# Kernel optimization log

Measured on AMD Instinct MI355X. Metric: run time of the kernel, lower is better.

The kernel has to match this reference:

```python
import jax, jax.numpy as jnp
import numpy as np

D_ATOM, D_MODEL, H = 128, 512, 4
D_H = D_ATOM // H
D_FF = 4 * D_ATOM
EPS = 1e-5


def _ln(x, g, b):
    m = jnp.mean(x, axis=-1, keepdims=True)
    v = jnp.mean((x - m) ** 2, axis=-1, keepdims=True)
    return (x - m) / jnp.sqrt(v + EPS) * g + b


def setup_inputs() -> dict:
    key = jax.random.key(0)
    ks = jax.random.split(key, 20)
    B, N_ATOM, N_PAIRS, N_TOK = 2, 2048, 16384, 512
    c_atom = jax.random.normal(ks[0], (B, N_ATOM, D_ATOM), dtype=jnp.float32)
    p_lm = jax.random.normal(ks[1], (B, N_PAIRS, 16), dtype=jnp.float32)
    p_lm_idx = jax.random.randint(ks[2], (B, N_PAIRS, 2), 0, N_ATOM, dtype=jnp.int32)
    token_idx = jnp.sort(jax.random.randint(ks[3], (B, N_ATOM), 0, N_TOK, dtype=jnp.int32), axis=-1)
    s = 0.05
    w = lambda k, sh: jax.random.normal(k, sh, dtype=jnp.float32) * s
    return {
        'c_atom': c_atom, 'p_lm': p_lm, 'p_lm_idx': p_lm_idx,
        'token_idx': token_idx, 'n_tokens': N_TOK,
        'ln_attn_g': jnp.ones((D_ATOM,), jnp.float32), 'ln_attn_b': jnp.zeros((D_ATOM,), jnp.float32),
        'w_q': w(ks[4], (D_ATOM, D_ATOM)), 'w_k': w(ks[5], (D_ATOM, D_ATOM)),
        'w_v': w(ks[6], (D_ATOM, D_ATOM)), 'w_g': w(ks[7], (D_ATOM, D_ATOM)),
        'w_o': w(ks[8], (D_ATOM, D_ATOM)),
        'pb_w': w(ks[9], (16, H)), 'pb_b': jnp.zeros((H,), jnp.float32),
        'ln_ff_g': jnp.ones((D_ATOM,), jnp.float32), 'ln_ff_b': jnp.zeros((D_ATOM,), jnp.float32),
        'sw_w1': w(ks[10], (D_ATOM, D_FF)), 'sw_w2': w(ks[11], (D_ATOM, D_FF)),
        'sw_w3': w(ks[12], (D_FF, D_ATOM)),
        'tok_w': w(ks[13], (D_ATOM, D_MODEL)), 'tok_b': jnp.zeros((D_MODEL,), jnp.float32),
    }


def reference(c_atom, p_lm, p_lm_idx, token_idx, n_tokens,
              ln_attn_g, ln_attn_b, w_q, w_k, w_v, w_g, w_o, pb_w, pb_b,
              ln_ff_g, ln_ff_b, sw_w1, sw_w2, sw_w3, tok_w, tok_b):
    B, N, _ = c_atom.shape
    q_n = _ln(c_atom, ln_attn_g, ln_attn_b)
    Q = (q_n @ w_q).reshape(B, N, H, D_H)
    K = (q_n @ w_k).reshape(B, N, H, D_H)
    V = (q_n @ w_v).reshape(B, N, H, D_H)
    G = q_n @ w_g  # (B, N, d_atom)

    scores = jnp.einsum('bihd,bjhd->bhij', Q, K) / jnp.sqrt(jnp.float32(D_H))

    bias = p_lm @ pb_w + pb_b  # (B, P, H)
    def scat(src, dst, b_):
        return jnp.zeros((H, N, N), b_.dtype).at[:, src, dst].set(b_.T)
    pair_bias = jax.vmap(scat)(p_lm_idx[..., 0], p_lm_idx[..., 1], bias)
    scores = scores + pair_bias

    token_mask = token_idx[:, :, None] == token_idx[:, None, :]  # (B,N,N)
    scores = jnp.where(token_mask[:, None], scores, -jnp.inf)
    attn = jax.nn.softmax(scores, axis=-1)
    attn = jnp.nan_to_num(attn)

    att_out = jnp.einsum('bhij,bjhd->bihd', attn, V).reshape(B, N, D_ATOM)
    q = c_atom + jax.nn.sigmoid(G) * (att_out @ w_o)
    h = _ln(q, ln_ff_g, ln_ff_b)
    q = q + (jax.nn.silu(h @ sw_w1) * (h @ sw_w2)) @ sw_w3
    atom_feat = q @ tok_w + tok_b  # (B, N, d_model)

    seg = (token_idx + jnp.arange(B, dtype=token_idx.dtype)[:, None] * n_tokens).reshape(-1)
    sums = jax.ops.segment_sum(atom_feat.reshape(B * N, D_MODEL), seg, num_segments=B * n_tokens)
    cnts = jax.ops.segment_sum(jnp.ones((B * N,), atom_feat.dtype), seg, num_segments=B * n_tokens)
    out = sums / jnp.maximum(cnts, 1.0)[:, None]
    return out.reshape(B, n_tokens, D_MODEL)
```

## Files before the change

kernel.cpp:

```cpp
#include <hip/hip_runtime.h>
#include <hip/hip_bf16.h>
#include <math.h>

#define B_     2
#define N_     2048
#define DA     128
#define H_     4
#define DH     32
#define DFF    512
#define DM     512
#define NT     512
#define NP     16384
#define MAXL   32
#define LDSP   136
#define PVS    40

typedef short bf16x8 __attribute__((ext_vector_type(8)));
typedef float f32x4  __attribute__((ext_vector_type(4)));

__device__ __forceinline__ short bf16r(float x) {
    union { float f; unsigned u; } v; v.f = x;
    unsigned r = v.u + 0x7FFFu + ((v.u >> 16) & 1u);
    return (short)(r >> 16);
}
__device__ __forceinline__ float bf2f(short h) {
    union { unsigned u; float f; } v;
    v.u = ((unsigned)(unsigned short)h) << 16;
    return v.f;
}

__global__ __launch_bounds__(1024) void setup_kernel(
        const float* __restrict__ wq, const float* __restrict__ wk,
        const float* __restrict__ wv, const float* __restrict__ wg,
        const float* __restrict__ wo, const float* __restrict__ w1,
        const float* __restrict__ w2, const float* __restrict__ w3,
        const float* __restrict__ tw, const int* __restrict__ tok,
        const int* __restrict__ pidx,
        const float* __restrict__ c_atom, const float* __restrict__ lng,
        const float* __restrict__ lnb,
        short* __restrict__ pqkvg, short* __restrict__ pwo,
        short* __restrict__ pw12, short* __restrict__ pw3,
        short* __restrict__ ptok, short* __restrict__ hln,
        int* __restrict__ cnt, int* __restrict__ tst,
        int* __restrict__ win) {
    __shared__ int c[1024];
    __shared__ int sb[1024];
    if (blockIdx.x < 42) {
        int gid = blockIdx.x * 1024 + threadIdx.x;
        int lane = gid & 63;
        int grp = gid >> 6;
        int quad = lane >> 4, nn = lane & 15;
        const float* src; short* dst; int stride;
        if (grp < 128) {
            int g = grp; int kt = g & 3, nt = g >> 2;
            int n = nt * 16 + nn;
            const float* w = (n < 128) ? wq : (n < 256) ? wk : (n < 384) ? wv : wg;
            src = w + (kt * 32 + quad * 8) * 128 + (n & 127);
            dst = pqkvg + (g * 64 + lane) * 8;
            stride = 128;
        } else if (grp < 160) {
            int g = grp - 128; int kt = g & 3, nt = g >> 2;
            src = wo + (kt * 32 + quad * 8) * 128 + nt * 16 + nn;
            dst = pwo + (g * 64 + lane) * 8;
            stride = 128;
        } else if (grp < 416) {
            int g = grp - 160; int kt = g & 3, nt = g >> 2;
            int n = nt * 16 + nn;
            src = ((n & 1) ? w2 : w1) + (kt * 32 + quad * 8) * 512 + (n >> 1);
            dst = pw12 + (g * 64 + lane) * 8;
            stride = 512;
        } else if (grp < 544) {
            int g = grp - 416; int kt = g & 15, nt = g >> 4;
            src = w3 + (kt * 32 + quad * 8) * 128 + nt * 16 + nn;
            dst = pw3 + (g * 64 + lane) * 8;
            stride = 128;
        } else {
            int g = grp - 544; int kt = g & 3, nt = g >> 2;
            src = tw + (kt * 32 + quad * 8) * 512 + nt * 16 + nn;
            dst = ptok + (g * 64 + lane) * 8;
            stride = 512;
        }
#pragma unroll
        for (int j = 0; j < 8; j++) dst[j] = bf16r(src[j * stride]);
    } else if (blockIdx.x == 42) {
        int tid = threadIdx.x;
        c[tid] = 0;
        __syncthreads();
#pragma unroll
        for (int i = 0; i < 4; i++) {
            int idx = tid + i * 1024;
            int b = idx >> 11;
            atomicAdd(&c[b * NT + tok[idx]], 1);
        }
        __syncthreads();
        int t = tid & (NT - 1);
        int v = c[tid];
        int* cur = c;
        int* alt = sb;
        for (int d = 1; d < NT; d <<= 1) {
            int y = cur[tid];
            if (t >= d) y += cur[tid - d];
            alt[tid] = y;
            __syncthreads();
            int* tmp = cur; cur = alt; alt = tmp;
        }
        tst[tid] = cur[tid] - v;
        cnt[tid] = v;
    } else if (blockIdx.x < 75) {
        int p = (blockIdx.x - 43) * 1024 + threadIdx.x;
        int b = p >> 14, pp = p & (NP - 1);
        int src = pidx[p * 2], dst = pidx[p * 2 + 1];
        if (tok[b * N_ + src] == tok[b * N_ + dst])
            atomicMax(&win[(b * N_ + src) * MAXL + (dst & 31)], pp + 1);
    } else {
        int t = threadIdx.x;
        int rowg = (blockIdx.x - 75) * 256 + (t >> 2);
        int sub = t & 3;
        const float* xr = c_atom + rowg * DA + sub * 32;
        float4 v[8];
        float s = 0.f, sq = 0.f;
#pragma unroll
        for (int i = 0; i < 8; i++) {
            v[i] = *(const float4*)(xr + i * 4);
            s  += v[i].x + v[i].y + v[i].z + v[i].w;
            sq += v[i].x * v[i].x + v[i].y * v[i].y + v[i].z * v[i].z + v[i].w * v[i].w;
        }
        s += __shfl_xor(s, 1); sq += __shfl_xor(sq, 1);
        s += __shfl_xor(s, 2); sq += __shfl_xor(sq, 2);
        float mean = s * (1.f / 128.f);
        float var = sq * (1.f / 128.f) - mean * mean;
        float inv = rsqrtf(var + 1e-5f);
        const float* gp = lng + sub * 32;
        const float* bp = lnb + sub * 32;
        short* dst = hln + rowg * DA + sub * 32;
#pragma unroll
        for (int i = 0; i < 8; i++) {
            dst[i * 4 + 0] = bf16r((v[i].x - mean) * inv * gp[i * 4 + 0] + bp[i * 4 + 0]);
            dst[i * 4 + 1] = bf16r((v[i].y - mean) * inv * gp[i * 4 + 1] + bp[i * 4 + 1]);
            dst[i * 4 + 2] = bf16r((v[i].z - mean) * inv * gp[i * 4 + 2] + bp[i * 4 + 2]);
            dst[i * 4 + 3] = bf16r((v[i].w - mean) * inv * gp[i * 4 + 3] + bp[i * 4 + 3]);
        }
    }
}

template<int KT, int KTB, int NTT, int STR>
__device__ __forceinline__ void gemm_a(const short* __restrict__ Abase,
                                       const short* __restrict__ Bp,
                                       int nt0, int lane, f32x4* acc) {
    const short* arow = Abase + (lane & 15) * STR + (lane >> 4) * 8;
    const short* bbase = Bp + lane * 8;
#pragma unroll
    for (int kt = 0; kt < KT; kt++) {
        bf16x8 a = *(const bf16x8*)(arow + kt * 32);
#pragma unroll
        for (int nt = 0; nt < NTT; nt++) {
            bf16x8 b = *(const bf16x8*)(bbase + ((nt0 + nt) * KTB + kt) * 512);
            acc[nt] = __builtin_amdgcn_mfma_f32_16x16x32_bf16(a, b, acc[nt], 0, 0, 0);
        }
    }
}

__global__ __launch_bounds__(256, 2) void tokfused(
        const short* __restrict__ hln, const float* __restrict__ c_atom,
        const float* __restrict__ plm,
        const int* __restrict__ tst, const int* __restrict__ cnt,
        const int* __restrict__ win,
        const short* __restrict__ pqkvg, const short* __restrict__ pwo,
        const short* __restrict__ pw12, const short* __restrict__ pw3,
        const short* __restrict__ ptok,
        const float* __restrict__ pbw, const float* __restrict__ pbb,
        const float* __restrict__ lnfg, const float* __restrict__ lnfb,
        const float* __restrict__ tb, float* __restrict__ out) {
    __shared__ __align__(16) char arena[54272];
    short* As  = (short*)(arena + 0);
    short* Qs  = (short*)(arena + 8704);
    short* Ps  = (short*)(arena + 8704);
    short* Ks  = (short*)(arena + 18944);
    short* VT  = (short*)(arena + 27648);
    float* sgf = (float*)(arena + 37888);
    float* valf = (float*)(arena + 8704);
    short* us   = (short*)(arena + 27648);
    short* q2s  = (short*)(arena + 0);
    short* mrs  = (short*)(arena + 25088);

    int token = blockIdx.x;
    int b = token >> 9;
    int tid = threadIdx.x;
    int lane = tid & 63, wave = tid >> 6;
    int quad = lane >> 4, cc = lane & 15;
    int start = tst[token];
    int L = cnt[token]; if (L > MAXL) L = MAXL;

    {
        int row = tid >> 3, sub = tid & 7;
        int4 v0 = {0,0,0,0}, v1 = {0,0,0,0};
        if (row < L) {
            const int4* src = (const int4*)(hln + (size_t)(b * N_ + start + row) * DA + sub * 16);
            v0 = src[0]; v1 = src[1];
        }
        int4* dst = (int4*)(As + row * LDSP + sub * 16);
        dst[0] = v0; dst[1] = v1;
    }
    __syncthreads();

    {
        f32x4 a0[8], a1[8];
#pragma unroll
        for (int i = 0; i < 8; i++)
#pragma unroll
            for (int r = 0; r < 4; r++) { a0[i][r] = 0.f; a1[i][r] = 0.f; }
        gemm_a<4, 4, 8, LDSP>(As, pqkvg, wave * 8, lane, a0);
        gemm_a<4, 4, 8, LDSP>(As + 16 * LDSP, pqkvg, wave * 8, lane, a1);
#pragma unroll
        for (int rt = 0; rt < 2; rt++) {
            f32x4* ac = rt ? a1 : a0;
#pragma unroll
            for (int nt = 0; nt < 8; nt++) {
                int lc = nt * 16 + cc;
#pragma unroll
                for (int r = 0; r < 4; r++) {
                    int lrow = rt * 16 + quad * 4 + r;
                    float v = ac[nt][r];
                    if (wave == 3)      sgf[lrow * 128 + lc] = 1.f / (1.f + expf(-v));
                    else if (wave == 0) Qs[lrow * LDSP + lc] = bf16r(v);
                    else if (wave == 1) Ks[lrow * LDSP + lc] = bf16r(v);
                    else VT[(lc >> 5) * 32 * PVS + (lc & 31) * PVS + lrow] = bf16r(v);
                }
            }
        }
    }
    __syncthreads();

    {
        int h = wave;
        const float scale = 0.17677669529663687f;
        int rb = lane & 15;
        bf16x8 qa0 = *(const bf16x8*)(Qs + rb * LDSP + h * 32 + quad * 8);
        bf16x8 qa1 = *(const bf16x8*)(Qs + (16 + rb) * LDSP + h * 32 + quad * 8);
        bf16x8 kb0 = *(const bf16x8*)(Ks + rb * LDSP + h * 32 + quad * 8);
        bf16x8 kb1 = *(const bf16x8*)(Ks + (16 + rb) * LDSP + h * 32 + quad * 8);
        f32x4 z = {0.f, 0.f, 0.f, 0.f};
        f32x4 sc[2][2];
        sc[0][0] = __builtin_amdgcn_mfma_f32_16x16x32_bf16(qa0, kb0, z, 0, 0, 0);
        sc[0][1] = __builtin_amdgcn_mfma_f32_16x16x32_bf16(qa0, kb1, z, 0, 0, 0);
        sc[1][0] = __builtin_amdgcn_mfma_f32_16x16x32_bf16(qa1, kb0, z, 0, 0, 0);
        sc[1][1] = __builtin_amdgcn_mfma_f32_16x16x32_bf16(qa1, kb1, z, 0, 0, 0);
        __syncthreads();
        short* Ph = Ps + h * 32 * PVS;
        int j0 = cc, j1 = 16 + cc;
#pragma unroll
        for (int it = 0; it < 2; it++) {
#pragma unroll
            for (int r = 0; r < 4; r++) {
                int i = it * 16 + quad * 4 + r;
                int at = start + i; if (at > N_ - 1) at = N_ - 1;
                const int* wrow = win + (size_t)(b * N_ + at) * MAXL;
                float s0 = sc[it][0][r] * scale;
                float s1 = sc[it][1][r] * scale;
                int pw0 = (j0 < L) ? wrow[(start + j0) & 31] : 0;
                int pw1 = (j1 < L) ? wrow[(start + j1) & 31] : 0;
                if (pw0 > 0) {
                    const float* pl = plm + (size_t)(b * NP + pw0 - 1) * 16;
                    float bs = pbb[h];
#pragma unroll
                    for (int f = 0; f < 16; f++) bs += pl[f] * pbw[f * H_ + h];
                    s0 += bs;
                }
                if (pw1 > 0) {
                    const float* pl = plm + (size_t)(b * NP + pw1 - 1) * 16;
                    float bs = pbb[h];
#pragma unroll
                    for (int f = 0; f < 16; f++) bs += pl[f] * pbw[f * H_ + h];
                    s1 += bs;
                }
                if (j0 >= L) s0 = -1e30f;
                if (j1 >= L) s1 = -1e30f;
                float m = fmaxf(s0, s1);
                m = fmaxf(m, __shfl_xor(m, 1));
                m = fmaxf(m, __shfl_xor(m, 2));
                m = fmaxf(m, __shfl_xor(m, 4));
                m = fmaxf(m, __shfl_xor(m, 8));
                float e0 = expf(s0 - m), e1 = expf(s1 - m);
                float sm = e0 + e1;
                sm += __shfl_xor(sm, 1);
                sm += __shfl_xor(sm, 2);
                sm += __shfl_xor(sm, 4);
                sm += __shfl_xor(sm, 8);
                float inv = 1.f / sm;
                Ph[i * PVS + j0] = bf16r(e0 * inv);
                Ph[i * PVS + j1] = bf16r(e1 * inv);
            }
        }
        __syncthreads();
        const short* Vh = VT + h * 32 * PVS;
        bf16x8 va0 = *(const bf16x8*)(Vh + rb * PVS + quad * 8);
        bf16x8 va1 = *(const bf16x8*)(Vh + (16 + rb) * PVS + quad * 8);
        bf16x8 pb0 = *(const bf16x8*)(Ph + rb * PVS + quad * 8);
        bf16x8 pb1 = *(const bf16x8*)(Ph + (16 + rb) * PVS + quad * 8);
        f32x4 ot[2][2];
        ot[0][0] = __builtin_amdgcn_mfma_f32_16x16x32_bf16(va0, pb0, z, 0, 0, 0);
        ot[0][1] = __builtin_amdgcn_mfma_f32_16x16x32_bf16(va0, pb1, z, 0, 0, 0);
        ot[1][0] = __builtin_amdgcn_mfma_f32_16x16x32_bf16(va1, pb0, z, 0, 0, 0);
        ot[1][1] = __builtin_amdgcn_mfma_f32_16x16x32_bf16(va1, pb1, z, 0, 0, 0);
#pragma unroll
        for (int dt = 0; dt < 2; dt++)
#pragma unroll
            for (int itile = 0; itile < 2; itile++)
#pragma unroll
                for (int r = 0; r < 4; r++)
                    As[(itile * 16 + cc) * LDSP + h * 32 + dt * 16 + quad * 4 + r] =
                        bf16r(ot[dt][itile][r]);
    }
    __syncthreads();

    {
        f32x4 a3[4];
#pragma unroll
        for (int i = 0; i < 4; i++)
#pragma unroll
            for (int r = 0; r < 4; r++) a3[i][r] = 0.f;
        gemm_a<4, 4, 4, LDSP>(As + (wave >> 1) * 16 * LDSP, pwo, (wave & 1) * 4, lane, a3);
#pragma unroll
        for (int ntl = 0; ntl < 4; ntl++) {
            int gcol = ((wave & 1) * 4 + ntl) * 16 + cc;
#pragma unroll
            for (int r = 0; r < 4; r++) {
                int lrow = (wave >> 1) * 16 + quad * 4 + r;
                int garow = start + lrow; if (garow > N_ - 1) garow = N_ - 1;
                float v = c_atom[(size_t)(b * N_ + garow) * DA + gcol]
                        + sgf[lrow * 128 + gcol] * a3[ntl][r];
                valf[lrow * 128 + gcol] = v;
            }
        }
    }
    __syncthreads();

    {
        int row = tid >> 3, sub = tid & 7;
        const float* vr = valf + row * 128 + sub * 16;
        float4 x[4];
        float s = 0.f, sq = 0.f;
#pragma unroll
        for (int i = 0; i < 4; i++) {
            x[i] = *(const float4*)(vr + i * 4);
            s  += x[i].x + x[i].y + x[i].z + x[i].w;
            sq += x[i].x * x[i].x + x[i].y * x[i].y + x[i].z * x[i].z + x[i].w * x[i].w;
        }
        s += __shfl_xor(s, 1); sq += __shfl_xor(sq, 1);
        s += __shfl_xor(s, 2); sq += __shfl_xor(sq, 2);
        s += __shfl_xor(s, 4); sq += __shfl_xor(sq, 4);
        float mean = s * (1.f / 128.f);
        float var = sq * (1.f / 128.f) - mean * mean;
        float inv = rsqrtf(var + 1e-5f);
        short* hr = As + row * LDSP + sub * 16;
        const float* gp = lnfg + sub * 16;
        const float* bp = lnfb + sub * 16;
#pragma unroll
        for (int i = 0; i < 4; i++) {
            hr[i * 4 + 0] = bf16r((x[i].x - mean) * inv * gp[i * 4 + 0] + bp[i * 4 + 0]);
            hr[i * 4 + 1] = bf16r((x[i].y - mean) * inv * gp[i * 4 + 1] + bp[i * 4 + 1]);
            hr[i * 4 + 2] = bf16r((x[i].z - mean) * inv * gp[i * 4 + 2] + bp[i * 4 + 2]);
            hr[i * 4 + 3] = bf16r((x[i].w - mean) * inv * gp[i * 4 + 3] + bp[i * 4 + 3]);
        }
    }
    __syncthreads();

    f32x4 c3a[4];
#pragma unroll
    for (int i = 0; i < 4; i++)
#pragma unroll
        for (int r = 0; r < 4; r++) c3a[i][r] = 0.f;
#pragma unroll
    for (int ch = 0; ch < 2; ch++) {
        f32x4 u0[8], u1[8];
#pragma unroll
        for (int i = 0; i < 8; i++)
#pragma unroll
            for (int r = 0; r < 4; r++) { u0[i][r] = 0.f; u1[i][r] = 0.f; }
        const short* bp12 = pw12 + ch * 32 * 4 * 512;
        gemm_a<4, 4, 8, LDSP>(As, bp12, wave * 8, lane, u0);
        gemm_a<4, 4, 8, LDSP>(As + 16 * LDSP, bp12, wave * 8, lane, u1);
#pragma unroll
        for (int rt = 0; rt < 2; rt++) {
            f32x4* ac = rt ? u1 : u0;
#pragma unroll
            for (int nt = 0; nt < 8; nt++) {
                int col8 = (wave * 8 + nt) * 8 + (cc >> 1);
#pragma unroll
                for (int r = 0; r < 4; r++) {
                    float v = ac[nt][r];
                    float p = __shfl_xor(v, 1);
                    if (!(lane & 1)) {
                        float sil = v / (1.f + expf(-v));
                        us[(rt * 16 + quad * 4 + r) * 264 + col8] = bf16r(sil * p);
                    }
                }
            }
        }
        __syncthreads();
        gemm_a<8, 16, 4, 264>(us + (wave >> 1) * 16 * 264, pw3 + ch * 8 * 512,
                              (wave & 1) * 4, lane, c3a);
        __syncthreads();
    }

    {
#pragma unroll
        for (int ntl = 0; ntl < 4; ntl++) {
            int gcol = ((wave & 1) * 4 + ntl) * 16 + cc;
#pragma unroll
            for (int r = 0; r < 4; r++) {
                int lrow = (wave >> 1) * 16 + quad * 4 + r;
                q2s[lrow * 128 + gcol] = bf16r(valf[lrow * 128 + gcol] + c3a[ntl][r]);
            }
        }
    }
    __syncthreads();

    if (tid < 128) {
        int col = tid;
        float sum = 0.f;
        for (int i = 0; i < L; i++) sum += bf2f(q2s[i * 128 + col]);
        float inv = (L > 0) ? 1.f / (float)L : 0.f;
        mrs[col] = bf16r(sum * inv);
    }
    __syncthreads();

    {
        f32x4 a8[8];
#pragma unroll
        for (int i = 0; i < 8; i++)
#pragma unroll
            for (int r = 0; r < 4; r++) a8[i][r] = 0.f;
        gemm_a<4, 4, 8, LDSP>(mrs, ptok, wave * 8, lane, a8);
        if (quad == 0) {
#pragma unroll
            for (int nt = 0; nt < 8; nt++) {
                int col = (wave * 8 + nt) * 16 + cc;
                out[(size_t)token * DM + col] = a8[nt][0] + tb[col];
            }
        }
    }
}

extern "C" void kernel_launch(void* const* d_in, const int* in_sizes, int n_in,
                              void* d_out, int out_size, void* d_ws, size_t ws_size,
                              hipStream_t stream) {
    const float* c_atom  = (const float*)d_in[0];
    const float* p_lm    = (const float*)d_in[1];
    const int*   p_idx   = (const int*)d_in[2];
    const int*   tok     = (const int*)d_in[3];
    const float* ln_a_g  = (const float*)d_in[5];
    const float* ln_a_b  = (const float*)d_in[6];
    const float* w_q     = (const float*)d_in[7];
    const float* w_k     = (const float*)d_in[8];
    const float* w_v     = (const float*)d_in[9];
    const float* w_g     = (const float*)d_in[10];
    const float* w_o     = (const float*)d_in[11];
    const float* pb_w    = (const float*)d_in[12];
    const float* pb_b    = (const float*)d_in[13];
    const float* ln_f_g  = (const float*)d_in[14];
    const float* ln_f_b  = (const float*)d_in[15];
    const float* sw_w1   = (const float*)d_in[16];
    const float* sw_w2   = (const float*)d_in[17];
    const float* sw_w3   = (const float*)d_in[18];
    const float* tok_w   = (const float*)d_in[19];
    const float* tok_b   = (const float*)d_in[20];
    float* out = (float*)d_out;

    float* ws = (float*)d_ws;
    int*   cnt   = (int*)ws;
    int*   tst   = cnt + 1024;
    int*   win   = tst + 1024;
    short* pqkvg = (short*)(win + 131072);
    short* pwo   = pqkvg + 65536;
    short* pw12  = pwo + 16384;
    short* pw3   = pw12 + 131072;
    short* ptok  = pw3 + 65536;
    short* hln   = ptok + 65536;

    setup_kernel<<<91, 1024, 0, stream>>>(w_q, w_k, w_v, w_g, w_o, sw_w1, sw_w2,
                                          sw_w3, tok_w, tok, p_idx,
                                          c_atom, ln_a_g, ln_a_b,
                                          pqkvg, pwo, pw12, pw3, ptok, hln,
                                          cnt, tst, win);

    tokfused<<<dim3(B_ * NT), dim3(256), 0, stream>>>(
        hln, c_atom, p_lm, tst, cnt, win,
        pqkvg, pwo, pw12, pw3, ptok,
        pb_w, pb_b, ln_f_g, ln_f_b, tok_b, out);
}
```

Baseline: 200.0 us.

## Precompute pair-bias table and add a fast path for short tokens

A new kernel computes the per-head pair-bias projection once per surviving pair and writes it into a windowed table indexed by atom and slot. The fused token kernel then reads that table instead of recomputing a 16-term dot product inside the softmax loop. For tokens with at most 16 atoms, a fast path skips the second 16-row tile in the QKVG, attention, output-projection, LayerNorm and SwiGLU stages, and zeroes the V buffer so the unused rows are clean. Exact expf is also swapped for __expf. The trade-offs are an extra launch, workspace for the bias table, and slightly lower precision in the sigmoid, softmax and SiLU exponentials.

```diff
diff --git a/kernel.cpp b/kernel.cpp
--- a/kernel.cpp
+++ b/kernel.cpp
@@ -143,6 +143,27 @@
     }
 }
 
+__global__ __launch_bounds__(1024) void biasfill(
+        const int* __restrict__ pidx, const int* __restrict__ tok,
+        const int* __restrict__ win, const float* __restrict__ plm,
+        const float* __restrict__ pbw, const float* __restrict__ pbb,
+        float* __restrict__ biasT) {
+    int p = blockIdx.x * 1024 + threadIdx.x;
+    int b = p >> 14, pp = p & (NP - 1);
+    int src = pidx[p * 2], dst = pidx[p * 2 + 1];
+    if (tok[b * N_ + src] != tok[b * N_ + dst]) return;
+    int key = (b * N_ + src) * MAXL + (dst & 31);
+    if (win[key] != pp + 1) return;
+    const float* pl = plm + (size_t)p * 16;
+#pragma unroll
+    for (int h = 0; h < H_; h++) {
+        float bs = pbb[h];
+#pragma unroll
+        for (int f = 0; f < 16; f++) bs += pl[f] * pbw[f * H_ + h];
+        biasT[(size_t)key * 4 + h] = bs;
+    }
+}
+
 template<int KT, int KTB, int NTT, int STR>
 __device__ __forceinline__ void gemm_a(const short* __restrict__ Abase,
                                        const short* __restrict__ Bp,
@@ -162,13 +183,12 @@
 
 __global__ __launch_bounds__(256, 2) void tokfused(
         const short* __restrict__ hln, const float* __restrict__ c_atom,
-        const float* __restrict__ plm,
+        const float* __restrict__ biasT,
         const int* __restrict__ tst, const int* __restrict__ cnt,
         const int* __restrict__ win,
         const short* __restrict__ pqkvg, const short* __restrict__ pwo,
         const short* __restrict__ pw12, const short* __restrict__ pw3,
         const short* __restrict__ ptok,
-        const float* __restrict__ pbw, const float* __restrict__ pbb,
         const float* __restrict__ lnfg, const float* __restrict__ lnfb,
         const float* __restrict__ tb, float* __restrict__ out) {
     __shared__ __align__(16) char arena[54272];
@@ -190,6 +210,7 @@
     int quad = lane >> 4, cc = lane & 15;
     int start = tst[token];
     int L = cnt[token]; if (L > MAXL) L = MAXL;
+    const bool fast = (L <= 16);
 
     {
         int row = tid >> 3, sub = tid & 7;
@@ -200,6 +221,15 @@
         }
         int4* dst = (int4*)(As + row * LDSP + sub * 16);
         dst[0] = v0; dst[1] = v1;
+        if (fast) {
+            int4* vz = (int4*)(arena + 27648);
+            int4 zz = {0,0,0,0};
+#pragma unroll
+            for (int k = 0; k < 3; k++) {
+                int idx = tid + k * 256;
+                if (idx < 640) vz[idx] = zz;
+            }
+        }
     }
     __syncthreads();
 
@@ -210,9 +240,10 @@
 #pragma unroll
             for (int r = 0; r < 4; r++) { a0[i][r] = 0.f; a1[i][r] = 0.f; }
         gemm_a<4, 4, 8, LDSP>(As, pqkvg, wave * 8, lane, a0);
-        gemm_a<4, 4, 8, LDSP>(As + 16 * LDSP, pqkvg, wave * 8, lane, a1);
+        if (!fast) gemm_a<4, 4, 8, LDSP>(As + 16 * LDSP, pqkvg, wave * 8, lane, a1);
 #pragma unroll
         for (int rt = 0; rt < 2; rt++) {
+            if (rt == 1 && fast) break;
             f32x4* ac = rt ? a1 : a0;
 #pragma unroll
             for (int nt = 0; nt < 8; nt++) {
@@ -221,7 +252,7 @@
                 for (int r = 0; r < 4; r++) {
                     int lrow = rt * 16 + quad * 4 + r;
                     float v = ac[nt][r];
-                    if (wave == 3)      sgf[lrow * 128 + lc] = 1.f / (1.f + expf(-v));
+                    if (wave == 3)      sgf[lrow * 128 + lc] = 1.f / (1.f + __expf(-v));
                     else if (wave == 0) Qs[lrow * LDSP + lc] = bf16r(v);
                     else if (wave == 1) Ks[lrow * LDSP + lc] = bf16r(v);
                     else VT[(lc >> 5) * 32 * PVS + (lc & 31) * PVS + lrow] = bf16r(v);
@@ -235,52 +266,48 @@
         int h = wave;
         const float scale = 0.17677669529663687f;
         int rb = lane & 15;
+        f32x4 z = {0.f, 0.f, 0.f, 0.f};
         bf16x8 qa0 = *(const bf16x8*)(Qs + rb * LDSP + h * 32 + quad * 8);
-        bf16x8 qa1 = *(const bf16x8*)(Qs + (16 + rb) * LDSP + h * 32 + quad * 8);
         bf16x8 kb0 = *(const bf16x8*)(Ks + rb * LDSP + h * 32 + quad * 8);
-        bf16x8 kb1 = *(const bf16x8*)(Ks + (16 + rb) * LDSP + h * 32 + quad * 8);
-        f32x4 z = {0.f, 0.f, 0.f, 0.f};
-        f32x4 sc[2][2];
-        sc[0][0] = __builtin_amdgcn_mfma_f32_16x16x32_bf16(qa0, kb0, z, 0, 0, 0);
-        sc[0][1] = __builtin_amdgcn_mfma_f32_16x16x32_bf16(qa0, kb1, z, 0, 0, 0);
-        sc[1][0] = __builtin_amdgcn_mfma_f32_16x16x32_bf16(qa1, kb0, z, 0, 0, 0);
-        sc[1][1] = __builtin_amdgcn_mfma_f32_16x16x32_bf16(qa1, kb1, z, 0, 0, 0);
+        f32x4 sc00 = __builtin_amdgcn_mfma_f32_16x16x32_bf16(qa0, kb0, z, 0, 0, 0);
+        f32x4 sc01 = z, sc10 = z, sc11 = z;
+        if (!fast) {
+            bf16x8 qa1 = *(const bf16x8*)(Qs + (16 + rb) * LDSP + h * 32 + quad * 8);
+            bf16x8 kb1 = *(const bf16x8*)(Ks + (16 + rb) * LDSP + h * 32 + quad * 8);
+            sc01 = __builtin_amdgcn_mfma_f32_16x16x32_bf16(qa0, kb1, z, 0, 0, 0);
+            sc10 = __builtin_amdgcn_mfma_f32_16x16x32_bf16(qa1, kb0, z, 0, 0, 0);
+            sc11 = __builtin_amdgcn_mfma_f32_16x16x32_bf16(qa1, kb1, z, 0, 0, 0);
+        }
         __syncthreads();
         short* Ph = Ps + h * 32 * PVS;
         int j0 = cc, j1 = 16 + cc;
 #pragma unroll
         for (int it = 0; it < 2; it++) {
+            if (it == 1 && fast) break;
+            f32x4 sj0 = it ? sc10 : sc00;
+            f32x4 sj1 = it ? sc11 : sc01;
 #pragma unroll
             for (int r = 0; r < 4; r++) {
                 int i = it * 16 + quad * 4 + r;
                 int at = start + i; if (at > N_ - 1) at = N_ - 1;
                 const int* wrow = win + (size_t)(b * N_ + at) * MAXL;
-                float s0 = sc[it][0][r] * scale;
-                float s1 = sc[it][1][r] * scale;
+                const float* brow = biasT + (size_t)(b * N_ + at) * MAXL * 4;
+                float s0 = sj0[r] * scale;
+                float s1 = fast ? -1e30f : sj1[r] * scale;
                 int pw0 = (j0 < L) ? wrow[(start + j0) & 31] : 0;
-                int pw1 = (j1 < L) ? wrow[(start + j1) & 31] : 0;
-                if (pw0 > 0) {
-                    const float* pl = plm + (size_t)(b * NP + pw0 - 1) * 16;
-                    float bs = pbb[h];
-#pragma unroll
-                    for (int f = 0; f < 16; f++) bs += pl[f] * pbw[f * H_ + h];
-                    s0 += bs;
-                }
-                if (pw1 > 0) {
-                    const float* pl = plm + (size_t)(b * NP + pw1 - 1) * 16;
-                    float bs = pbb[h];
-#pragma unroll
-                    for (int f = 0; f < 16; f++) bs += pl[f] * pbw[f * H_ + h];
-                    s1 += bs;
+                if (pw0 > 0) s0 += brow[((start + j0) & 31) * 4 + h];
+                if (!fast) {
+                    int pw1 = (j1 < L) ? wrow[(start + j1) & 31] : 0;
+                    if (pw1 > 0) s1 += brow[((start + j1) & 31) * 4 + h];
+                    if (j1 >= L) s1 = -1e30f;
                 }
                 if (j0 >= L) s0 = -1e30f;
-                if (j1 >= L) s1 = -1e30f;
                 float m = fmaxf(s0, s1);
                 m = fmaxf(m, __shfl_xor(m, 1));
                 m = fmaxf(m, __shfl_xor(m, 2));
                 m = fmaxf(m, __shfl_xor(m, 4));
                 m = fmaxf(m, __shfl_xor(m, 8));
-                float e0 = expf(s0 - m), e1 = expf(s1 - m);
+                float e0 = __expf(s0 - m), e1 = __expf(s1 - m);
                 float sm = e0 + e1;
                 sm += __shfl_xor(sm, 1);
                 sm += __shfl_xor(sm, 2);
@@ -296,24 +323,27 @@
         bf16x8 va0 = *(const bf16x8*)(Vh + rb * PVS + quad * 8);
         bf16x8 va1 = *(const bf16x8*)(Vh + (16 + rb) * PVS + quad * 8);
         bf16x8 pb0 = *(const bf16x8*)(Ph + rb * PVS + quad * 8);
-        bf16x8 pb1 = *(const bf16x8*)(Ph + (16 + rb) * PVS + quad * 8);
-        f32x4 ot[2][2];
-        ot[0][0] = __builtin_amdgcn_mfma_f32_16x16x32_bf16(va0, pb0, z, 0, 0, 0);
-        ot[0][1] = __builtin_amdgcn_mfma_f32_16x16x32_bf16(va0, pb1, z, 0, 0, 0);
-        ot[1][0] = __builtin_amdgcn_mfma_f32_16x16x32_bf16(va1, pb0, z, 0, 0, 0);
-        ot[1][1] = __builtin_amdgcn_mfma_f32_16x16x32_bf16(va1, pb1, z, 0, 0, 0);
-#pragma unroll
-        for (int dt = 0; dt < 2; dt++)
-#pragma unroll
-            for (int itile = 0; itile < 2; itile++)
-#pragma unroll
-                for (int r = 0; r < 4; r++)
-                    As[(itile * 16 + cc) * LDSP + h * 32 + dt * 16 + quad * 4 + r] =
-                        bf16r(ot[dt][itile][r]);
-    }
-    __syncthreads();
-
-    {
+        f32x4 ot00 = __builtin_amdgcn_mfma_f32_16x16x32_bf16(va0, pb0, z, 0, 0, 0);
+        f32x4 ot10 = __builtin_amdgcn_mfma_f32_16x16x32_bf16(va1, pb0, z, 0, 0, 0);
+#pragma unroll
+        for (int r = 0; r < 4; r++) {
+            As[cc * LDSP + h * 32 + quad * 4 + r]      = bf16r(ot00[r]);
+            As[cc * LDSP + h * 32 + 16 + quad * 4 + r] = bf16r(ot10[r]);
+        }
+        if (!fast) {
+            bf16x8 pb1 = *(const bf16x8*)(Ph + (16 + rb) * PVS + quad * 8);
+            f32x4 ot01 = __builtin_amdgcn_mfma_f32_16x16x32_bf16(va0, pb1, z, 0, 0, 0);
+            f32x4 ot11 = __builtin_amdgcn_mfma_f32_16x16x32_bf16(va1, pb1, z, 0, 0, 0);
+#pragma unroll
+            for (int r = 0; r < 4; r++) {
+                As[(16 + cc) * LDSP + h * 32 + quad * 4 + r]      = bf16r(ot01[r]);
+                As[(16 + cc) * LDSP + h * 32 + 16 + quad * 4 + r] = bf16r(ot11[r]);
+            }
+        }
+    }
+    __syncthreads();
+
+    if (!fast || wave < 2) {
         f32x4 a3[4];
 #pragma unroll
         for (int i = 0; i < 4; i++)
@@ -337,30 +367,32 @@
 
     {
         int row = tid >> 3, sub = tid & 7;
-        const float* vr = valf + row * 128 + sub * 16;
-        float4 x[4];
-        float s = 0.f, sq = 0.f;
-#pragma unroll
-        for (int i = 0; i < 4; i++) {
-            x[i] = *(const float4*)(vr + i * 4);
-            s  += x[i].x + x[i].y + x[i].z + x[i].w;
-            sq += x[i].x * x[i].x + x[i].y * x[i].y + x[i].z * x[i].z + x[i].w * x[i].w;
-        }
-        s += __shfl_xor(s, 1); sq += __shfl_xor(sq, 1);
-        s += __shfl_xor(s, 2); sq += __shfl_xor(sq, 2);
-        s += __shfl_xor(s, 4); sq += __shfl_xor(sq, 4);
-        float mean = s * (1.f / 128.f);
-        float var = sq * (1.f / 128.f) - mean * mean;
-        float inv = rsqrtf(var + 1e-5f);
-        short* hr = As + row * LDSP + sub * 16;
-        const float* gp = lnfg + sub * 16;
-        const float* bp = lnfb + sub * 16;
-#pragma unroll
-        for (int i = 0; i < 4; i++) {
-            hr[i * 4 + 0] = bf16r((x[i].x - mean) * inv * gp[i * 4 + 0] + bp[i * 4 + 0]);
-            hr[i * 4 + 1] = bf16r((x[i].y - mean) * inv * gp[i * 4 + 1] + bp[i * 4 + 1]);
-            hr[i * 4 + 2] = bf16r((x[i].z - mean) * inv * gp[i * 4 + 2] + bp[i * 4 + 2]);
-            hr[i * 4 + 3] = bf16r((x[i].w - mean) * inv * gp[i * 4 + 3] + bp[i * 4 + 3]);
+        if (!fast || row < 16) {
+            const float* vr = valf + row * 128 + sub * 16;
+            float4 x[4];
+            float s = 0.f, sq = 0.f;
+#pragma unroll
+            for (int i = 0; i < 4; i++) {
+                x[i] = *(const float4*)(vr + i * 4);
+                s  += x[i].x + x[i].y + x[i].z + x[i].w;
+                sq += x[i].x * x[i].x + x[i].y * x[i].y + x[i].z * x[i].z + x[i].w * x[i].w;
+            }
+            s += __shfl_xor(s, 1); sq += __shfl_xor(sq, 1);
+            s += __shfl_xor(s, 2); sq += __shfl_xor(sq, 2);
+            s += __shfl_xor(s, 4); sq += __shfl_xor(sq, 4);
+            float mean = s * (1.f / 128.f);
+            float var = sq * (1.f / 128.f) - mean * mean;
+            float inv = rsqrtf(var + 1e-5f);
+            short* hr = As + row * LDSP + sub * 16;
+            const float* gp = lnfg + sub * 16;
+            const float* bp = lnfb + sub * 16;
+#pragma unroll
+            for (int i = 0; i < 4; i++) {
+                hr[i * 4 + 0] = bf16r((x[i].x - mean) * inv * gp[i * 4 + 0] + bp[i * 4 + 0]);
+                hr[i * 4 + 1] = bf16r((x[i].y - mean) * inv * gp[i * 4 + 1] + bp[i * 4 + 1]);
+                hr[i * 4 + 2] = bf16r((x[i].z - mean) * inv * gp[i * 4 + 2] + bp[i * 4 + 2]);
+                hr[i * 4 + 3] = bf16r((x[i].w - mean) * inv * gp[i * 4 + 3] + bp[i * 4 + 3]);
+            }
         }
     }
     __syncthreads();
@@ -379,9 +411,10 @@
             for (int r = 0; r < 4; r++) { u0[i][r] = 0.f; u1[i][r] = 0.f; }
         const short* bp12 = pw12 + ch * 32 * 4 * 512;
         gemm_a<4, 4, 8, LDSP>(As, bp12, wave * 8, lane, u0);
-        gemm_a<4, 4, 8, LDSP>(As + 16 * LDSP, bp12, wave * 8, lane, u1);
+        if (!fast) gemm_a<4, 4, 8, LDSP>(As + 16 * LDSP, bp12, wave * 8, lane, u1);
 #pragma unroll
         for (int rt = 0; rt < 2; rt++) {
+            if (rt == 1 && fast) break;
             f32x4* ac = rt ? u1 : u0;
 #pragma unroll
             for (int nt = 0; nt < 8; nt++) {
@@ -391,19 +424,20 @@
                     float v = ac[nt][r];
                     float p = __shfl_xor(v, 1);
                     if (!(lane & 1)) {
-                        float sil = v / (1.f + expf(-v));
+                        float sil = v / (1.f + __expf(-v));
                         us[(rt * 16 + quad * 4 + r) * 264 + col8] = bf16r(sil * p);
                     }
                 }
             }
         }
         __syncthreads();
-        gemm_a<8, 16, 4, 264>(us + (wave >> 1) * 16 * 264, pw3 + ch * 8 * 512,
-                              (wave & 1) * 4, lane, c3a);
+        if (!fast || wave < 2)
+            gemm_a<8, 16, 4, 264>(us + (wave >> 1) * 16 * 264, pw3 + ch * 8 * 512,
+                                  (wave & 1) * 4, lane, c3a);
         __syncthreads();
     }
 
-    {
+    if (!fast || wave < 2) {
 #pragma unroll
         for (int ntl = 0; ntl < 4; ntl++) {
             int gcol = ((wave & 1) * 4 + ntl) * 16 + cc;
@@ -477,6 +511,7 @@
     short* pw3   = pw12 + 131072;
     short* ptok  = pw3 + 65536;
     short* hln   = ptok + 65536;
+    float* biasT = (float*)(hln + 524288);
 
     setup_kernel<<<91, 1024, 0, stream>>>(w_q, w_k, w_v, w_g, w_o, sw_w1, sw_w2,
                                           sw_w3, tok_w, tok, p_idx,
@@ -484,8 +519,10 @@
                                           pqkvg, pwo, pw12, pw3, ptok, hln,
                                           cnt, tst, win);
 
+    biasfill<<<32, 1024, 0, stream>>>(p_idx, tok, win, p_lm, pb_w, pb_b, biasT);
+
     tokfused<<<dim3(B_ * NT), dim3(256), 0, stream>>>(
-        hln, c_atom, p_lm, tst, cnt, win,
+        hln, c_atom, biasT, tst, cnt, win,
         pqkvg, pwo, pw12, pw3, ptok,
-        pb_w, pb_b, ln_f_g, ln_f_b, tok_b, out);
-}
+        ln_f_g, ln_f_b, tok_b, out);
+}
```

Result: faster. 166.0 us (-17.0%).
